# Kernel optimization log

Measured on AMD Instinct MI355X. Metric: run time of the kernel, lower is better.

## Reference

```python
import jax, jax.numpy as jnp
import numpy as np

N_EMBD = 384
N_HEADS = 6
HEAD_SIZE = N_EMBD // N_HEADS  # 64
D_FF = 4 * N_EMBD
EPS = 1e-5


def layernorm(x, g, b):
    mu = jnp.mean(x, axis=-1, keepdims=True)
    var = jnp.var(x, axis=-1, keepdims=True)
    return (x - mu) * jax.lax.rsqrt(var + EPS) * g + b


def setup_inputs() -> dict:
    key = jax.random.key(0)
    ks = jax.random.split(key, 12)
    B, T, C, H, HS = 64, 256, N_EMBD, N_HEADS, HEAD_SIZE
    s = 0.02
    return {
        "x": jax.random.normal(ks[0], (B, T, C), jnp.float32),
        "Wq": jax.random.normal(ks[1], (H, C, HS), jnp.float32) * s,
        "Wk": jax.random.normal(ks[2], (H, C, HS), jnp.float32) * s,
        "Wv": jax.random.normal(ks[3], (H, C, HS), jnp.float32) * s,
        "Wo": jax.random.normal(ks[4], (C, C), jnp.float32) * s,
        "bo": jnp.zeros((C,), jnp.float32),
        "W1": jax.random.normal(ks[5], (C, D_FF), jnp.float32) * s,
        "b1": jnp.zeros((D_FF,), jnp.float32),
        "W2": jax.random.normal(ks[6], (D_FF, C), jnp.float32) * s,
        "b2": jnp.zeros((C,), jnp.float32),
        "g1": jnp.ones((C,), jnp.float32),
        "beta1": jnp.zeros((C,), jnp.float32),
        "g2": jnp.ones((C,), jnp.float32),
        "beta2": jnp.zeros((C,), jnp.float32),
    }


def reference(x, Wq, Wk, Wv, Wo, bo, W1, b1, W2, b2, g1, beta1, g2, beta2):
    B, T, C = x.shape
    # --- attention branch (dropout = identity in eval) ---
    h = layernorm(x, g1, beta1)
    q = jnp.einsum('btc,hck->bhtk', h, Wq)
    k = jnp.einsum('btc,hck->bhtk', h, Wk)
    v = jnp.einsum('btc,hck->bhtk', h, Wv)
    scale = HEAD_SIZE ** -0.5
    wei = jnp.einsum('bhtk,bhsk->bhts', q, k) * scale  # [B,H,T,T]
    causal = jnp.tril(jnp.ones((T, T), bool))
    wei = jnp.where(causal, wei, -jnp.inf)
    wei = jax.nn.softmax(wei, axis=-1)
    attn = jnp.einsum('bhts,bhsk->bthk', wei, v).reshape(B, T, C)
    x = x + attn @ Wo + bo
    # --- MLP branch ---
    h2 = layernorm(x, g2, beta2)
    ff = jax.nn.relu(h2 @ W1 + b1) @ W2 + b2
    return x + ff
```

## Files before the change

kernel.cpp:

```cpp
#include <hip/hip_runtime.h>

#define B 64
#define T 256
#define C 384
#define H 6
#define HS 64
#define DFF 1536
#define BT (B*T)

typedef __attribute__((ext_vector_type(8))) short short8;
typedef __attribute__((ext_vector_type(4))) float float4v;
typedef __attribute__((ext_vector_type(4))) unsigned short ushort4v;

static __device__ __forceinline__ unsigned short f2bf(float f) {
  unsigned int u = __float_as_uint(f);
  unsigned int r = (u + 0x7fffu + ((u >> 16) & 1u)) >> 16;
  return (unsigned short)r;
}

typedef __attribute__((address_space(1))) const unsigned int ga_u32;
typedef __attribute__((address_space(3))) unsigned int ls_u32;
static __device__ __forceinline__ void gld16(const void* g, void* l) {
  __builtin_amdgcn_global_load_lds((ga_u32*)g, (ls_u32*)l, 16, 0, 0);
}

__global__ __launch_bounds__(256) void prep_w(
    const float* __restrict__ Wq, const float* __restrict__ Wk, const float* __restrict__ Wv,
    const float* __restrict__ Wo, const float* __restrict__ W1, const float* __restrict__ W2,
    unsigned short* __restrict__ wqkv, unsigned short* __restrict__ wo,
    unsigned short* __restrict__ w1t, unsigned short* __restrict__ w2t) {
  __shared__ float tile[32][33];
  int bx = blockIdx.x;
  int x = threadIdx.x & 31, y = threadIdx.x >> 5;
  if (bx < 432) {
    int tn = bx % 36, tc = bx / 36;
    int n0 = tn * 32, c0 = tc * 32;
    int mat = n0 / 384, rem = n0 % 384, head = rem / 64, hs0 = rem % 64;
    const float* W = (mat == 0) ? Wq : ((mat == 1) ? Wk : Wv);
    const float* src = W + (size_t)head * C * HS + hs0;
    #pragma unroll
    for (int i = 0; i < 4; ++i) tile[y + 8 * i][x] = src[(size_t)(c0 + y + 8 * i) * 64 + x];
    __syncthreads();
    #pragma unroll
    for (int i = 0; i < 4; ++i)
      wqkv[(size_t)(n0 + y + 8 * i) * 384 + c0 + x] = f2bf(tile[x][y + 8 * i]);
    return;
  }
  const float* src; unsigned short* dst; int CN, R, n0, c0;
  if (bx < 576) {
    int t = bx - 432; n0 = (t % 12) * 32; c0 = (t / 12) * 32;
    src = Wo; dst = wo; CN = 384; R = 384;
  } else if (bx < 1152) {
    int t = bx - 576; n0 = (t % 48) * 32; c0 = (t / 48) * 32;
    src = W1; dst = w1t; CN = 1536; R = 384;
  } else {
    int t = bx - 1152; n0 = (t % 12) * 32; c0 = (t / 12) * 32;
    src = W2; dst = w2t; CN = 384; R = 1536;
  }
  #pragma unroll
  for (int i = 0; i < 4; ++i) tile[y + 8 * i][x] = src[(size_t)(c0 + y + 8 * i) * CN + n0 + x];
  __syncthreads();
  #pragma unroll
  for (int i = 0; i < 4; ++i)
    dst[(size_t)(n0 + y + 8 * i) * R + c0 + x] = f2bf(tile[x][y + 8 * i]);
}

__global__ __launch_bounds__(256) void ln_kernel(const float* __restrict__ x,
    const float* __restrict__ g, const float* __restrict__ bta,
    unsigned short* __restrict__ out) {
  int t = blockIdx.x * 4 + (threadIdx.x >> 6);
  int lane = threadIdx.x & 63;
  const float* row = x + (size_t)t * C;
  float v[6];
  float s = 0.f, ss = 0.f;
  #pragma unroll
  for (int i = 0; i < 6; ++i) {
    v[i] = row[lane + i * 64];
    s += v[i];
    ss += v[i] * v[i];
  }
  #pragma unroll
  for (int m = 32; m >= 1; m >>= 1) {
    s += __shfl_xor(s, m);
    ss += __shfl_xor(ss, m);
  }
  float mu = s / C;
  float var = ss / C - mu * mu;
  float rstd = rsqrtf(var + 1e-5f);
  unsigned short* orow = out + (size_t)t * C;
  #pragma unroll
  for (int i = 0; i < 6; ++i) {
    int c = lane + i * 64;
    orow[c] = f2bf((v[i] - mu) * rstd * g[c] + bta[c]);
  }
}

template<int EPI, int MT>
__global__ __launch_bounds__(MT >= 256 ? 512 : 256) void gemm_kernel(
    const unsigned short* __restrict__ A, const unsigned short* __restrict__ Wt,
    const float* __restrict__ bias, const float* __restrict__ resid,
    float* __restrict__ outf,
    unsigned short* __restrict__ outb, unsigned short* __restrict__ outb2,
    unsigned short* __restrict__ outb3, int K, int N) {
  __shared__ unsigned short Ash[MT * 64];
  __shared__ unsigned short Bsh[128 * 64];
  constexpr int NW = (MT >= 256) ? 8 : 4;
  constexpr int WM = NW / 2;
  constexpr int MR = MT / WM / 16;
  constexpr int NA = (MT / 8) / NW;
  constexpr int NB = 16 / NW;
  int tid = threadIdx.x, lane = tid & 63, w = tid >> 6;
  int wm = w >> 1, wn = w & 1;
  int bxs = ((blockIdx.x & 7) * (gridDim.x >> 3)) + (blockIdx.x >> 3);
  int m0 = bxs * MT, n0 = blockIdx.y * 128;
  int lrow = lane >> 3;
  int lchunk = (lane & 7) ^ (lrow & 7);
  int frow = lane & 15, cg = lane >> 4;
  float4v acc[MR][4] = {};
  for (int k0 = 0; k0 < K; k0 += 64) {
    __syncthreads();
    #pragma unroll
    for (int i = 0; i < NA; ++i) {
      int win = w * NA + i;
      gld16(A + (size_t)(m0 + win * 8 + lrow) * K + k0 + lchunk * 8, &Ash[win * 512]);
    }
    #pragma unroll
    for (int i = 0; i < NB; ++i) {
      int win = w * NB + i;
      gld16(Wt + (size_t)(n0 + win * 8 + lrow) * K + k0 + lchunk * 8, &Bsh[win * 512]);
    }
    __syncthreads();
    #pragma unroll
    for (int ks = 0; ks < 2; ++ks) {
      short8 af[MR], bf[4];
      #pragma unroll
      for (int mi = 0; mi < MR; ++mi) {
        int r = wm * (MR * 16) + mi * 16 + frow;
        int ch = (ks * 4 + cg) ^ (r & 7);
        af[mi] = *(const short8*)((const char*)Ash + r * 128 + ch * 16);
      }
      #pragma unroll
      for (int ni = 0; ni < 4; ++ni) {
        int r = wn * 64 + ni * 16 + frow;
        int ch = (ks * 4 + cg) ^ (r & 7);
        bf[ni] = *(const short8*)((const char*)Bsh + r * 128 + ch * 16);
      }
      #pragma unroll
      for (int mi = 0; mi < MR; ++mi)
        #pragma unroll
        for (int ni = 0; ni < 4; ++ni)
          acc[mi][ni] = __builtin_amdgcn_mfma_f32_16x16x32_bf16(af[mi], bf[ni], acc[mi][ni], 0, 0, 0);
    }
  }
  int cl = lane & 15;
  #pragma unroll
  for (int mi = 0; mi < MR; ++mi) {
    #pragma unroll
    for (int ni = 0; ni < 4; ++ni) {
      if constexpr (EPI == 0) {
        int gc = n0 + wn * 64 + ni * 16 + cl;
        int mat = gc / 384;
        int head = (gc % 384) >> 6;
        int hs = gc & 63;
        int gr0 = m0 + wm * (MR * 16) + mi * 16 + cg * 4;
        int tt0 = gr0 & 255, bidx = gr0 >> 8;
        size_t bhb = (size_t)(bidx * H + head);
        if (mat == 2) {
          ushort4v pk;
          #pragma unroll
          for (int j = 0; j < 4; ++j) pk[j] = f2bf(acc[mi][ni][j]);
          *(ushort4v*)&outb3[(bhb * HS + hs) * T + tt0] = pk;
        } else {
          unsigned short* dst = (mat == 0) ? outb : outb2;
          #pragma unroll
          for (int j = 0; j < 4; ++j)
            dst[(bhb * T + tt0 + j) * HS + hs] = f2bf(acc[mi][ni][j]);
        }
      } else {
        #pragma unroll
        for (int j = 0; j < 4; ++j) {
          int gr = m0 + wm * (MR * 16) + mi * 16 + cg * 4 + j;
          int gc = n0 + wn * 64 + ni * 16 + cl;
          float val = acc[mi][ni][j];
          if constexpr (EPI == 1) {
            size_t i = (size_t)gr * N + gc;
            outf[i] = resid[i] + val + bias[gc];
          } else if constexpr (EPI == 2) {
            outb[(size_t)gr * N + gc] = f2bf(fmaxf(val + bias[gc], 0.f));
          } else {
            size_t i = (size_t)gr * N + gc;
            outf[i] = resid[i] + val + bias[gc];
          }
        }
      }
    }
  }
}

__global__ __launch_bounds__(256) void attn_kernel(
    const unsigned short* __restrict__ qg, const unsigned short* __restrict__ kg,
    const unsigned short* __restrict__ vtg, unsigned short* __restrict__ ab) {
  __shared__ unsigned short Ksh[64 * 64];
  __shared__ unsigned short Vsh[64 * 256];
  __shared__ unsigned short Psh[4 * 16 * 256];
  int bh = blockIdx.x;
  int bb = bh / H, hh = bh % H;
  int qt = blockIdx.y, q0 = qt * 64;
  int tid = threadIdx.x, lane = tid & 63, w = tid >> 6;
  int cl = lane & 15, cg = lane >> 4;
  const float scale_log2e = 0.125f * 1.44269504f;
  const unsigned short* qp = qg + ((size_t)bh * T) * HS;
  const unsigned short* kp = kg + ((size_t)bh * T) * HS;
  const unsigned short* vp = vtg + ((size_t)bh * HS) * T;

  short8 aq[2];
  #pragma unroll
  for (int k0 = 0; k0 < 2; ++k0)
    aq[k0] = *(const short8*)&qp[(size_t)(q0 + w * 16 + cl) * HS + cg * 8 + k0 * 32];

  #pragma unroll
  for (int i = 0; i < 8; ++i) {
    int idx = tid + i * 256;
    int r = idx >> 5, c16 = idx & 31;
    uint4 val = *(const uint4*)&vp[(size_t)r * T + c16 * 8];
    int byte = (r * 512 + c16 * 16) ^ ((r & 7) << 4);
    *(uint4*)((char*)Vsh + byte) = val;
  }

  float4v sacc[4][4] = {};
  for (int si = 0; si <= qt; ++si) {
    __syncthreads();
    #pragma unroll
    for (int i = 0; i < 2; ++i) {
      int idx = tid + i * 256;
      int r = idx >> 3, c16 = idx & 7;
      uint4 val = *(const uint4*)&kp[(size_t)(si * 64 + r) * HS + c16 * 8];
      int byte = (r * 128 + c16 * 16) ^ ((r & 7) << 4);
      *(uint4*)((char*)Ksh + byte) = val;
    }
    __syncthreads();
    #pragma unroll
    for (int ss = 0; ss < 4; ++ss) {
      if (ss == si) {
        #pragma unroll
        for (int nt = 0; nt < 4; ++nt) {
          int srow = nt * 16 + cl;
          #pragma unroll
          for (int k0 = 0; k0 < 2; ++k0) {
            int byte = (srow * 128 + (cg * 8 + k0 * 32) * 2) ^ ((srow & 7) << 4);
            short8 bf = *(const short8*)((char*)Ksh + byte);
            sacc[ss][nt] = __builtin_amdgcn_mfma_f32_16x16x32_bf16(aq[k0], bf, sacc[ss][nt], 0, 0, 0);
          }
        }
      }
    }
  }

  #pragma unroll
  for (int si = 0; si < 4; ++si) {
    if (si == qt) {
      #pragma unroll
      for (int nt = 0; nt < 4; ++nt) {
        int s = q0 + nt * 16 + cl;
        #pragma unroll
        for (int j = 0; j < 4; ++j) {
          int q = q0 + w * 16 + cg * 4 + j;
          if (s > q) sacc[si][nt][j] = -1e30f;
        }
      }
    }
  }

  float lj[4];
  #pragma unroll
  for (int j = 0; j < 4; ++j) {
    float m = -1e30f;
    #pragma unroll
    for (int si = 0; si < 4; ++si) if (si <= qt)
      #pragma unroll
      for (int nt = 0; nt < 4; ++nt) m = fmaxf(m, sacc[si][nt][j]);
    #pragma unroll
    for (int off = 1; off < 16; off <<= 1) m = fmaxf(m, __shfl_xor(m, off));
    float l = 0.f;
    #pragma unroll
    for (int si = 0; si < 4; ++si) if (si <= qt)
      #pragma unroll
      for (int nt = 0; nt < 4; ++nt) {
        float p0 = exp2f((sacc[si][nt][j] - m) * scale_log2e);
        sacc[si][nt][j] = p0;
        l += p0;
      }
    #pragma unroll
    for (int off = 1; off < 16; off <<= 1) l += __shfl_xor(l, off);
    lj[j] = 1.f / l;
  }

  char* pbase = (char*)Psh + w * 8192;
  #pragma unroll
  for (int si = 0; si < 4; ++si) if (si <= qt)
    #pragma unroll
    for (int nt = 0; nt < 4; ++nt)
      #pragma unroll
      for (int j = 0; j < 4; ++j) {
        int prow = cg * 4 + j, col = si * 64 + nt * 16 + cl;
        int byte = (prow * 512 + col * 2) ^ ((prow & 7) << 4);
        *(unsigned short*)(pbase + byte) = f2bf(sacc[si][nt][j]);
      }

  int nks = 2 * (qt + 1);
  #pragma unroll
  for (int nt = 0; nt < 4; ++nt) {
    float4v oacc = {};
    for (int ks = 0; ks < nks; ++ks) {
      int k = ks * 32 + cg * 8;
      int pbyte = (cl * 512 + k * 2) ^ ((cl & 7) << 4);
      short8 af = *(const short8*)(pbase + pbyte);
      int vr = nt * 16 + cl;
      int vbyte = (vr * 512 + k * 2) ^ ((vr & 7) << 4);
      short8 bf = *(const short8*)((char*)Vsh + vbyte);
      oacc = __builtin_amdgcn_mfma_f32_16x16x32_bf16(af, bf, oacc, 0, 0, 0);
    }
    #pragma unroll
    for (int j = 0; j < 4; ++j) {
      int t = q0 + w * 16 + cg * 4 + j;
      ab[((size_t)(bb * T + t)) * C + hh * 64 + nt * 16 + cl] = f2bf(oacc[j] * lj[j]);
    }
  }
}

extern "C" void kernel_launch(void* const* d_in, const int* in_sizes, int n_in,
                              void* d_out, int out_size, void* d_ws, size_t ws_size,
                              hipStream_t stream) {
  const float* x   = (const float*)d_in[0];
  const float* Wq  = (const float*)d_in[1];
  const float* Wk  = (const float*)d_in[2];
  const float* Wv  = (const float*)d_in[3];
  const float* Wo  = (const float*)d_in[4];
  const float* bo  = (const float*)d_in[5];
  const float* W1  = (const float*)d_in[6];
  const float* b1  = (const float*)d_in[7];
  const float* W2  = (const float*)d_in[8];
  const float* b2  = (const float*)d_in[9];
  const float* g1  = (const float*)d_in[10];
  const float* be1 = (const float*)d_in[11];
  const float* g2  = (const float*)d_in[12];
  const float* be2 = (const float*)d_in[13];
  float* out = (float*)d_out;
  float* ws = (float*)d_ws;

  unsigned short* wqkv_t = (unsigned short*)ws;
  unsigned short* wo_t   = wqkv_t + 442368;
  unsigned short* w1t    = wo_t + 147456;
  unsigned short* w2t    = w1t + 589824;
  float* base2 = ws + 884736;
  unsigned short* h  = (unsigned short*)base2;
  float* x2 = base2 + 3145728;
  unsigned short* ab = (unsigned short*)(x2 + 6291456);
  unsigned short* qb = (unsigned short*)(x2 + 6291456 + 3145728);
  unsigned short* kb = qb + 6291456;
  unsigned short* vt = kb + 6291456;
  unsigned short* ffb = ab;

  prep_w<<<1728, 256, 0, stream>>>(Wq, Wk, Wv, Wo, W1, W2, wqkv_t, wo_t, w1t, w2t);
  ln_kernel<<<BT / 4, 256, 0, stream>>>(x, g1, be1, h);
  gemm_kernel<0, 256><<<dim3(64, 9), 512, 0, stream>>>(h, wqkv_t, nullptr, nullptr,
                                                       nullptr, qb, kb, vt, 384, 1152);
  attn_kernel<<<dim3(B * H, T / 64), 256, 0, stream>>>(qb, kb, vt, ab);
  gemm_kernel<1, 64><<<dim3(256, 3), 256, 0, stream>>>(ab, wo_t, bo, x,
                                                       x2, nullptr, nullptr, nullptr, 384, 384);
  ln_kernel<<<BT / 4, 256, 0, stream>>>(x2, g2, be2, h);
  gemm_kernel<2, 256><<<dim3(64, 12), 512, 0, stream>>>(h, w1t, b1, nullptr,
                                                        nullptr, ffb, nullptr, nullptr, 384, 1536);
  gemm_kernel<3, 64><<<dim3(256, 3), 256, 0, stream>>>(ffb, w2t, b2, x2,
                                                       out, nullptr, nullptr, nullptr, 1536, 384);
}
```

Before: 151.7 us.

## Fuse output projection with residual add and second LayerNorm

Adds a proj_ln_kernel in which each 512-thread block computes a full 64x384 row tile of the attention output projection. It adds the residual and bias, reduces row statistics across waves through shared memory, and writes both x2 and the bf16 LayerNorm output, replacing a separate GEMM plus LN launch and a round trip through x2. The grid is only 256 blocks with single-buffered loads, so parallelism and latency hiding are reduced. The final FFN down-projection also switches to the larger 256-row tile configuration with 512 threads.

```diff
diff --git a/kernel.cpp b/kernel.cpp
--- a/kernel.cpp
+++ b/kernel.cpp
@@ -182,10 +182,7 @@
           int gr = m0 + wm * (MR * 16) + mi * 16 + cg * 4 + j;
           int gc = n0 + wn * 64 + ni * 16 + cl;
           float val = acc[mi][ni][j];
-          if constexpr (EPI == 1) {
-            size_t i = (size_t)gr * N + gc;
-            outf[i] = resid[i] + val + bias[gc];
-          } else if constexpr (EPI == 2) {
+          if constexpr (EPI == 2) {
             outb[(size_t)gr * N + gc] = f2bf(fmaxf(val + bias[gc], 0.f));
           } else {
             size_t i = (size_t)gr * N + gc;
@@ -193,6 +190,88 @@
           }
         }
       }
+    }
+  }
+}
+
+__global__ __launch_bounds__(512) void proj_ln_kernel(
+    const unsigned short* __restrict__ A, const unsigned short* __restrict__ Wt,
+    const float* __restrict__ bo, const float* __restrict__ x,
+    const float* __restrict__ g2, const float* __restrict__ be2,
+    float* __restrict__ x2, unsigned short* __restrict__ h2) {
+  __shared__ unsigned short Ash[64 * 64];
+  __shared__ unsigned short Bsh[384 * 64];
+  __shared__ float red[64][2][2];
+  int tid = threadIdx.x, lane = tid & 63, w = tid >> 6;
+  int wm = w >> 1, wn = w & 1;
+  int bxs = ((blockIdx.x & 7) * (gridDim.x >> 3)) + (blockIdx.x >> 3);
+  int m0 = bxs * 64;
+  int lrow = lane >> 3;
+  int lchunk = (lane & 7) ^ (lrow & 7);
+  int frow = lane & 15, cg = lane >> 4, cl = lane & 15;
+  float4v acc[12] = {};
+  for (int k0 = 0; k0 < 384; k0 += 64) {
+    __syncthreads();
+    gld16(A + (size_t)(m0 + w * 8 + lrow) * 384 + k0 + lchunk * 8, &Ash[w * 512]);
+    #pragma unroll
+    for (int i = 0; i < 6; ++i) {
+      int win = w * 6 + i;
+      gld16(Wt + (size_t)(win * 8 + lrow) * 384 + k0 + lchunk * 8, &Bsh[win * 512]);
+    }
+    __syncthreads();
+    #pragma unroll
+    for (int ks = 0; ks < 2; ++ks) {
+      int ra = wm * 16 + frow;
+      int cha = (ks * 4 + cg) ^ (ra & 7);
+      short8 af = *(const short8*)((const char*)Ash + ra * 128 + cha * 16);
+      #pragma unroll
+      for (int nt = 0; nt < 12; ++nt) {
+        int rb = wn * 192 + nt * 16 + frow;
+        int chb = (ks * 4 + cg) ^ (rb & 7);
+        short8 bf = *(const short8*)((const char*)Bsh + rb * 128 + chb * 16);
+        acc[nt] = __builtin_amdgcn_mfma_f32_16x16x32_bf16(af, bf, acc[nt], 0, 0, 0);
+      }
+    }
+  }
+  #pragma unroll
+  for (int nt = 0; nt < 12; ++nt) {
+    int gc = wn * 192 + nt * 16 + cl;
+    #pragma unroll
+    for (int j = 0; j < 4; ++j) {
+      int gr = m0 + wm * 16 + cg * 4 + j;
+      acc[nt][j] += x[(size_t)gr * 384 + gc] + bo[gc];
+    }
+  }
+  __syncthreads();
+  #pragma unroll
+  for (int j = 0; j < 4; ++j) {
+    float s = 0.f, ss = 0.f;
+    #pragma unroll
+    for (int nt = 0; nt < 12; ++nt) { float v = acc[nt][j]; s += v; ss += v * v; }
+    #pragma unroll
+    for (int off = 1; off < 16; off <<= 1) { s += __shfl_xor(s, off); ss += __shfl_xor(ss, off); }
+    if (cl == 0) {
+      int lr = wm * 16 + cg * 4 + j;
+      red[lr][wn][0] = s;
+      red[lr][wn][1] = ss;
+    }
+  }
+  __syncthreads();
+  #pragma unroll
+  for (int j = 0; j < 4; ++j) {
+    int lr = wm * 16 + cg * 4 + j;
+    int gr = m0 + lr;
+    float s = red[lr][0][0] + red[lr][1][0];
+    float ss = red[lr][0][1] + red[lr][1][1];
+    float mu = s / 384.f;
+    float var = ss / 384.f - mu * mu;
+    float rstd = rsqrtf(var + 1e-5f);
+    #pragma unroll
+    for (int nt = 0; nt < 12; ++nt) {
+      int gc = wn * 192 + nt * 16 + cl;
+      float v = acc[nt][j];
+      x2[(size_t)gr * 384 + gc] = v;
+      h2[(size_t)gr * 384 + gc] = f2bf((v - mu) * rstd * g2[gc] + be2[gc]);
     }
   }
 }
@@ -366,11 +445,9 @@
   gemm_kernel<0, 256><<<dim3(64, 9), 512, 0, stream>>>(h, wqkv_t, nullptr, nullptr,
                                                        nullptr, qb, kb, vt, 384, 1152);
   attn_kernel<<<dim3(B * H, T / 64), 256, 0, stream>>>(qb, kb, vt, ab);
-  gemm_kernel<1, 64><<<dim3(256, 3), 256, 0, stream>>>(ab, wo_t, bo, x,
-                                                       x2, nullptr, nullptr, nullptr, 384, 384);
-  ln_kernel<<<BT / 4, 256, 0, stream>>>(x2, g2, be2, h);
+  proj_ln_kernel<<<256, 512, 0, stream>>>(ab, wo_t, bo, x, g2, be2, x2, h);
   gemm_kernel<2, 256><<<dim3(64, 12), 512, 0, stream>>>(h, w1t, b1, nullptr,
                                                         nullptr, ffb, nullptr, nullptr, 384, 1536);
-  gemm_kernel<3, 64><<<dim3(256, 3), 256, 0, stream>>>(ffb, w2t, b2, x2,
+  gemm_kernel<3, 256><<<dim3(64, 3), 512, 0, stream>>>(ffb, w2t, b2, x2,
                                                        out, nullptr, nullptr, nullptr, 1536, 384);
 }
```

After: 163.4 us. 1.08x slower.
